# Optimization experiments

Hardware: AMD Instinct MI355X
Metric: run time of the kernel (lower is better)

Reference implementation:

```python
import math
import jax, jax.numpy as jnp
import numpy as np

L, B = 576, 16           # residues, batch
HID, ALPHA = 800, 60     # lstm hidden, alphabet size
IN0, IN1 = 41, 2 * HID   # lstm layer input sizes (20 one-hot + 21 pssm)


def _unit(v):
    return v / jnp.linalg.norm(v, axis=-1, keepdims=True)


def _frame(a, b, c):
    # rotation matrix (columns) of the local reference frame at point c
    bc = _unit(c - b)
    n = _unit(jnp.cross(b - a, bc))
    return jnp.stack([bc, jnp.cross(n, bc), n], axis=-1)  # (..., 3, 3)


def _extend(a, b, c, ct):
    # place next atom given previous three atoms and SRF coordinates ct
    R = _frame(a, b, c)
    return c + jnp.einsum('...ij,...j->...i', R, ct)


def lstm_dir(x, w_ih, w_hh, b_ih, b_hh, reverse=False):
    # single-direction LSTM over x: (T, B, D); torch gate order i,f,g,o
    H = w_hh.shape[1]
    Bb = x.shape[1]

    def step(carry, xt):
        h, cst = carry
        gates = xt @ w_ih.T + b_ih + h @ w_hh.T + b_hh
        i, f, g, o = jnp.split(gates, 4, axis=-1)
        cnew = jax.nn.sigmoid(f) * cst + jax.nn.sigmoid(i) * jnp.tanh(g)
        hnew = jax.nn.sigmoid(o) * jnp.tanh(cnew)
        return (hnew, cnew), hnew

    zeros = jnp.zeros((Bb, H), x.dtype)
    _, hs = jax.lax.scan(step, (zeros, zeros), x, reverse=reverse)
    return hs  # (T, B, H), in original time order for both directions


def torsion_to_srf(r, theta, phi):
    # r, theta: (3,) fixed bond lengths/angles; phi: (L, B, 3) torsions
    r = r[None, None, :]
    th = theta[None, None, :]
    c = jnp.stack([r * jnp.cos(th) * jnp.ones_like(phi),
                   r * jnp.cos(phi) * jnp.sin(th),
                   r * jnp.sin(phi) * jnp.sin(th)], axis=-1)  # (L, B, 3, 3)
    Lx, Bx = phi.shape[0], phi.shape[1]
    return jnp.transpose(c, (0, 2, 1, 3)).reshape(3 * Lx, Bx, 3)


def pnerf(c_tilde, nfrag):
    # parallel NeRF: run nfrag fragments in parallel, then stitch sequentially
    A, Bb, _ = c_tilde.shape
    F = A // nfrag  # assumes divisibility (guaranteed by chosen L)
    c = c_tilde.reshape(nfrag, F, Bb, 3).transpose(1, 0, 2, 3).reshape(F, nfrag * Bb, 3)
    init = jnp.array([[-np.sqrt(0.5), np.sqrt(1.5), 0.0],
                      [-np.sqrt(2.0), 0.0, 0.0],
                      [0.0, 0.0, 0.0]], dtype=c_tilde.dtype)
    a0 = jnp.broadcast_to(init[0], (nfrag * Bb, 3))
    b0 = jnp.broadcast_to(init[1], (nfrag * Bb, 3))
    c0 = jnp.broadcast_to(init[2], (nfrag * Bb, 3))

    def step(carry, ct):
        a, b, cc = carry
        d = _extend(a, b, cc, ct)
        return (b, cc, d), d

    _, frag = jax.lax.scan(step, (a0, b0, c0), c)  # (F, nfrag*Bb, 3)
    frag = frag.reshape(F, nfrag, Bb, 3)

    coords = frag[:, 0]  # fragment 0 already in global frame
    for k in range(1, nfrag):  # small fixed loop over fragments
        R = _frame(coords[-3], coords[-2], coords[-1])  # (Bb, 3, 3)
        g = coords[-1][None] + jnp.einsum('bij,fbj->fbi', R, frag[:, k])
        coords = jnp.concatenate([coords, g], axis=0)
    return coords  # (3L, B, 3)


def _p(k, shape):
    return 0.05 * jax.random.normal(k, shape, dtype=jnp.float32)


def setup_inputs():
    key = jax.random.key(0)
    ks = jax.random.split(key, 32)
    inp = {}
    inp['seq'] = jax.random.randint(ks[0], (L, B), 0, 20)
    inp['pssm'] = jax.random.uniform(ks[1], (L, B, 21), dtype=jnp.float32)
    inp['length'] = jnp.full((B,), L, dtype=jnp.int32)  # full lengths (packing is a no-op)
    i = 2
    for layer, din in ((0, IN0), (1, IN1)):
        for d in ('f', 'b'):
            inp[f'w_ih_l{layer}{d}'] = _p(ks[i], (4 * HID, din)); i += 1
            inp[f'w_hh_l{layer}{d}'] = _p(ks[i], (4 * HID, HID)); i += 1
            inp[f'b_ih_l{layer}{d}'] = _p(ks[i], (4 * HID,)); i += 1
            inp[f'b_hh_l{layer}{d}'] = _p(ks[i], (4 * HID,)); i += 1
    inp['fc_w'] = _p(ks[i], (ALPHA, 2 * HID)); i += 1
    inp['fc_b'] = _p(ks[i], (ALPHA,)); i += 1
    inp['alphabet'] = jax.random.uniform(ks[i], (ALPHA, 3), minval=-math.pi, maxval=math.pi, dtype=jnp.float32); i += 1
    inp['bond_lengths'] = jnp.array([145.867432, 152.534744, 132.935516], dtype=jnp.float32)
    inp['bond_angles'] = jnp.array([1.019982, 1.20471, 1.109421], dtype=jnp.float32)
    return inp


def reference(seq, pssm, length,
              w_ih_l0f, w_hh_l0f, b_ih_l0f, b_hh_l0f,
              w_ih_l0b, w_hh_l0b, b_ih_l0b, b_hh_l0b,
              w_ih_l1f, w_hh_l1f, b_ih_l1f, b_hh_l1f,
              w_ih_l1b, w_hh_l1b, b_ih_l1b, b_hh_l1b,
              fc_w, fc_b, alphabet, bond_lengths, bond_angles):
    # eval mode: inter-layer dropout omitted; all lengths == L so packing is identity
    x = jnp.concatenate([jax.nn.one_hot(seq, 20, dtype=pssm.dtype), pssm], axis=-1)  # (L,B,41)
    h = jnp.concatenate([lstm_dir(x, w_ih_l0f, w_hh_l0f, b_ih_l0f, b_hh_l0f),
                         lstm_dir(x, w_ih_l0b, w_hh_l0b, b_ih_l0b, b_hh_l0b, reverse=True)], axis=-1)
    h = jnp.concatenate([lstm_dir(h, w_ih_l1f, w_hh_l1f, b_ih_l1f, b_hh_l1f),
                         lstm_dir(h, w_ih_l1b, w_hh_l1b, b_ih_l1b, b_hh_l1b, reverse=True)], axis=-1)
    p = jax.nn.softmax(h @ fc_w.T + fc_b, axis=-1)            # (L,B,ALPHA)
    phi = jnp.arctan2(p @ jnp.sin(alphabet), p @ jnp.cos(alphabet))  # (L,B,3)
    srf = torsion_to_srf(bond_lengths, bond_angles, phi)      # (3L,B,3)
    return pnerf(srf, int(math.sqrt(L)))                      # (3L,B,3)
```

## Files before the change

kernel.cpp:

```cpp
#include <hip/hip_runtime.h>
#include <hip/hip_fp16.h>

#define L_SEQ 576
#define BATCH 16
#define HIDDEN 800
#define NT 200
#define KQ_HH 25
#define KQ_L1 50
#define KQ_L0 2

typedef _Float16 h8 __attribute__((ext_vector_type(8)));
typedef _Float16 h4 __attribute__((ext_vector_type(4)));
typedef float f4 __attribute__((ext_vector_type(4)));
typedef int v4i __attribute__((ext_vector_type(4)));
typedef int v2i __attribute__((ext_vector_type(2)));

__device__ __forceinline__ float sigmoidf_(float x){
  x = fminf(30.f, fmaxf(-30.f, x));
  return 1.f/(1.f+__expf(-x));
}
__device__ __forceinline__ float tanhf_(float x){
  x = fminf(15.f, fmaxf(-15.f, x));
  float e = __expf(2.f*x);
  return (e-1.f)/(e+1.f);
}

__global__ void init_h(v4i* __restrict__ h){
  size_t i = (size_t)blockIdx.x*256 + threadIdx.x;
  v4i s = {0x7C007C00, 0x7C007C00, 0x7C007C00, 0x7C007C00};
  h[i] = s;
}

__global__ void build_x(const int* __restrict__ seq, const float* __restrict__ pssm,
                        _Float16* __restrict__ x){
  int i = blockIdx.x*256 + threadIdx.x;
  if(i >= L_SEQ*BATCH*64) return;
  int m = i >> 6, k = i & 63;
  float v = 0.f;
  if(k < 20)      v = (seq[m]==k) ? 1.f : 0.f;
  else if(k < 41) v = pssm[m*21 + (k-20)];
  x[i] = (_Float16)v;
}

__global__ void prep_w(
  const float* __restrict__ whh0f, const float* __restrict__ whh0b,
  const float* __restrict__ whh1f, const float* __restrict__ whh1b,
  const float* __restrict__ wih1f, const float* __restrict__ wih1b,
  const float* __restrict__ wih0f, const float* __restrict__ wih0b,
  h8* __restrict__ wp_hh, h8* __restrict__ wp1, h8* __restrict__ wp0)
{
  long idx = (long)blockIdx.x*256 + threadIdx.x;
  const long J1 = 4L*320000, J2 = 2L*640000, J3 = 2L*25600;
  if(idx < J1){
    int d = (int)(idx/320000); int r = (int)(idx%320000);
    int T = r/1600, q = (r%1600)/64, l = r&63;
    const float* W = (d==0)?whh0f:(d==1)?whh0b:(d==2)?whh1f:whh1b;
    int c = l&15; int n = (c&3)*800 + T*4 + (c>>2);
    const float* src = W + (size_t)n*800 + q*32 + ((l>>4)<<3);
    h8 v;
    #pragma unroll
    for(int j=0;j<8;++j) v[j] = (_Float16)src[j];
    wp_hh[idx] = v;
  } else if(idx < J1+J2){
    long i2 = idx - J1;
    int d = (int)(i2/640000); int r = (int)(i2%640000);
    int T = r/3200, q = (r%3200)/64, l = r&63;
    const float* W = d ? wih1b : wih1f;
    int c = l&15; int n = (c&3)*800 + T*4 + (c>>2);
    const float* src = W + (size_t)n*1600 + q*32 + ((l>>4)<<3);
    h8 v;
    #pragma unroll
    for(int j=0;j<8;++j) v[j] = (_Float16)src[j];
    wp1[i2] = v;
  } else if(idx < J1+J2+J3){
    long i3 = idx - J1 - J2;
    int d = (int)(i3/25600); int r = (int)(i3%25600);
    int T = r/128, q = (r%128)/64, l = r&63;
    const float* W = d ? wih0b : wih0f;
    int c = l&15; int n = (c&3)*800 + T*4 + (c>>2);
    int k0 = q*32 + ((l>>4)<<3);
    h8 v;
    #pragma unroll
    for(int j=0;j<8;++j){ int k = k0+j; v[j] = (_Float16)((k<41)? W[(size_t)n*41+k] : 0.f); }
    wp0[i3] = v;
  }
}

__global__ __launch_bounds__(256) void gemm_l0(
  const _Float16* __restrict__ A,
  const h8* __restrict__ WpF, const h8* __restrict__ WpB,
  const float* __restrict__ bihF, const float* __restrict__ bhhF,
  const float* __restrict__ bihB, const float* __restrict__ bhhB,
  _Float16* __restrict__ GpF, _Float16* __restrict__ GpB)
{
  const int wv = threadIdx.x >> 6;
  const int l  = threadIdx.x & 63;
  const int mg = blockIdx.x % 144;
  const int tg = blockIdx.x / 144;
  const int mt = mg*4 + wv;
  const int dir = tg / 50;
  const int Tb  = (tg % 50) * 4;
  const h8* Wp = dir ? WpB : WpF;
  const float* bih = dir ? bihB : bihF;
  const float* bhh = dir ? bhhB : bhhF;
  _Float16* Gp = dir ? GpB : GpF;

  const _Float16* ab = A + (size_t)(mt*16 + (l&15))*64 + ((l>>4)<<3);
  f4 acc[4] = {{0.f,0.f,0.f,0.f},{0.f,0.f,0.f,0.f},{0.f,0.f,0.f,0.f},{0.f,0.f,0.f,0.f}};
  for(int q=0;q<KQ_L0;++q){
    h8 av = *(const h8*)(ab + q*32);
    #pragma unroll
    for(int j=0;j<4;++j){
      h8 bv = Wp[((size_t)(Tb+j)*KQ_L0 + q)*64 + l];
      acc[j] = __builtin_amdgcn_mfma_f32_16x16x32_f16(bv, av, acc[j], 0, 0, 0);
    }
  }
  const int hi = l >> 4;
  #pragma unroll
  for(int j=0;j<4;++j){
    int T = Tb + j;
    int u = T*4 + hi;
    h4 o;
    #pragma unroll
    for(int r=0;r<4;++r){
      float bias = bih[r*800+u] + bhh[r*800+u];
      o[r] = (_Float16)(acc[j][r] + bias);
    }
    *(h4*)(Gp + (((size_t)mt*NT + T)*64 + l)*4) = o;
  }
}

__global__ __launch_bounds__(256) void gemm_l1(
  const h8* __restrict__ Af,
  const h8* __restrict__ WpF, const h8* __restrict__ WpB,
  const float* __restrict__ bihF, const float* __restrict__ bhhF,
  const float* __restrict__ bihB, const float* __restrict__ bhhB,
  _Float16* __restrict__ GpF, _Float16* __restrict__ GpB)
{
  __shared__ v4i ldsB[2][256];
  const int tid = threadIdx.x;
  const int wv = tid >> 6;
  const int l  = tid & 63;
  const int mg  = blockIdx.x % 36;
  const int tgd = blockIdx.x / 36;
  const int dir = tgd / 50;
  const int tg  = tgd % 50;
  const int Tb  = tg * 4;
  const int mtb = mg*16 + wv*4;
  const h8* Wp = dir ? WpB : WpF;
  const float* bih = dir ? bihB : bihF;
  const float* bhh = dir ? bhhB : bhhF;
  _Float16* Gp = dir ? GpB : GpF;

  const h8* a0 = Af + (size_t)(mtb+0)*3200 + l;
  const h8* a1 = Af + (size_t)(mtb+1)*3200 + l;
  const h8* a2 = Af + (size_t)(mtb+2)*3200 + l;
  const h8* a3 = Af + (size_t)(mtb+3)*3200 + l;

  f4 acc[4][4];
  #pragma unroll
  for(int m=0;m<4;++m)
    #pragma unroll
    for(int j=0;j<4;++j){ acc[m][j][0]=0.f; acc[m][j][1]=0.f; acc[m][j][2]=0.f; acc[m][j][3]=0.f; }

  {
    int j = tid >> 6, ll = tid & 63;
    ldsB[0][tid] = *(const v4i*)(Wp + ((size_t)(Tb+j)*KQ_L1 + 0)*64 + ll);
  }
  __syncthreads();
  for(int q=0;q<KQ_L1;++q){
    const int buf = q & 1;
    if(q+1 < KQ_L1){
      int j = tid >> 6, ll = tid & 63;
      ldsB[buf^1][tid] = *(const v4i*)(Wp + ((size_t)(Tb+j)*KQ_L1 + (q+1))*64 + ll);
    }
    h8 av0 = a0[q*64];
    h8 av1 = a1[q*64];
    h8 av2 = a2[q*64];
    h8 av3 = a3[q*64];
    #pragma unroll
    for(int j=0;j<4;++j){
      h8 bv = __builtin_bit_cast(h8, ldsB[buf][j*64 + l]);
      acc[0][j] = __builtin_amdgcn_mfma_f32_16x16x32_f16(bv, av0, acc[0][j], 0, 0, 0);
      acc[1][j] = __builtin_amdgcn_mfma_f32_16x16x32_f16(bv, av1, acc[1][j], 0, 0, 0);
      acc[2][j] = __builtin_amdgcn_mfma_f32_16x16x32_f16(bv, av2, acc[2][j], 0, 0, 0);
      acc[3][j] = __builtin_amdgcn_mfma_f32_16x16x32_f16(bv, av3, acc[3][j], 0, 0, 0);
    }
    __syncthreads();
  }
  const int hi = l >> 4;
  #pragma unroll
  for(int j=0;j<4;++j){
    int T = Tb + j;
    int u = T*4 + hi;
    float b0 = bih[0*800+u] + bhh[0*800+u];
    float b1 = bih[1*800+u] + bhh[1*800+u];
    float b2 = bih[2*800+u] + bhh[2*800+u];
    float b3 = bih[3*800+u] + bhh[3*800+u];
    #pragma unroll
    for(int m=0;m<4;++m){
      h4 o;
      o[0]=(_Float16)(acc[m][j][0]+b0); o[1]=(_Float16)(acc[m][j][1]+b1);
      o[2]=(_Float16)(acc[m][j][2]+b2); o[3]=(_Float16)(acc[m][j][3]+b3);
      *(h4*)(Gp + (((size_t)(mtb+m)*NT + T)*64 + l)*4) = o;
    }
  }
}

__global__ __launch_bounds__(256,1) void lstm_kernel(
  const h8* __restrict__ WpF, const h8* __restrict__ WpB,
  const _Float16* __restrict__ GpF, const _Float16* __restrict__ GpB,
  h8* __restrict__ hfrag)
{
  __shared__ __attribute__((aligned(16))) char lds_h[2*25600];
  const int tid = threadIdx.x;
  const int wv  = tid >> 6;
  const int l   = tid & 63;
  const bool bwd = blockIdx.x >= 50;
  const int T = ((bwd ? (int)blockIdx.x - 50 : (int)blockIdx.x) << 2) + wv;
  const h8* Wp = bwd ? WpB : WpF;
  const _Float16* Gp = bwd ? GpB : GpF;
  const int dirOff = bwd ? 1600 : 0;

  h8 Bf[KQ_HH];
  #pragma unroll
  for(int q=0;q<KQ_HH;++q) Bf[q] = Wp[(T*KQ_HH + q)*64 + l];

  float cs = 0.f;
  const int qb = wv*6;
  const int storeUnit = ((T>>3)<<6) + (((T>>1)&3)<<4);
  const int storeHalf = (T&1)<<3;

  for(int s=0; s<L_SEQ; ++s){
    const int t = bwd ? (L_SEQ-1-s) : s;

    h4 gp4 = *(const h4*)(Gp + (((size_t)t*NT + T)*64 + l)*4);

    #pragma unroll
    for(int q=0;q<KQ_HH;++q) asm volatile("" : "+v"(Bf[q]));

    char* lbuf = lds_h + (s&1)*25600;
    if(s > 0){
      const h8* src = hfrag + (size_t)(bwd ? t+1 : t-1)*3200 + dirOff + l;
      v4i w[7];
      for(;;){
        #pragma unroll
        for(int i=0;i<7;++i){
          unsigned long long ad = (unsigned long long)(src + (qb+i)*64);
          asm volatile("global_load_dwordx4 %0, %1, off sc1"
                       : "=v"(w[i]) : "v"(ad) : "memory");
        }
        asm volatile("s_waitcnt vmcnt(0)"
          : "+v"(w[0]),"+v"(w[1]),"+v"(w[2]),"+v"(w[3]),"+v"(w[4]),
            "+v"(w[5]),"+v"(w[6])
          :
          : "memory");
        int orac = 0;
        #pragma unroll
        for(int i=0;i<7;++i) orac |= (w[i][0]|w[i][1]) | (w[i][2]|w[i][3]);
        if(__all((orac & 0x40004000) == 0)) break;
        __builtin_amdgcn_s_sleep(1);
      }
      #pragma unroll
      for(int i=0;i<7;++i)
        *(v4i*)(lbuf + (qb+i)*1024 + l*16) = w[i];
    }
    __syncthreads();

    f4 acc[4];
    acc[0][0]=(float)gp4[0]; acc[0][1]=(float)gp4[1]; acc[0][2]=(float)gp4[2]; acc[0][3]=(float)gp4[3];
    #pragma unroll
    for(int j=1;j<4;++j){ acc[j][0]=0.f; acc[j][1]=0.f; acc[j][2]=0.f; acc[j][3]=0.f; }
    if(s > 0){
      #pragma unroll
      for(int q=0;q<KQ_HH;++q){
        v4i wq = *(const v4i*)(lbuf + q*1024 + l*16);
        acc[q&3] = __builtin_amdgcn_mfma_f32_16x16x32_f16(
                     Bf[q], __builtin_bit_cast(h8, wq), acc[q&3], 0,0,0);
      }
    }
    f4 g = (acc[0]+acc[1]) + (acc[2]+acc[3]);

    float cn = sigmoidf_(g[1])*cs + sigmoidf_(g[0])*tanhf_(g[2]);
    cs = cn;
    float hv = sigmoidf_(g[3])*tanhf_(cn);

    {
      _Float16 hf = (_Float16)hv;
      unsigned int u0 = (unsigned int)__builtin_bit_cast(unsigned short, hf);
      unsigned int up = (unsigned int)__shfl_xor((int)u0, 16, 64);
      unsigned int d01 = u0 | (up << 16);
      unsigned int d23 = (unsigned int)__shfl_xor((int)d01, 32, 64);
      if(l < 16){
        v2i ov; ov[0] = (int)d01; ov[1] = (int)d23;
        unsigned long long ad = (unsigned long long)
          ((char*)(hfrag + (size_t)t*3200 + dirOff + storeUnit + l) + storeHalf);
        asm volatile("global_store_dwordx2 %0, %1, off sc1" : : "v"(ad), "v"(ov) : "memory");
      }
    }
  }
}

__global__ void head_kernel(const h8* __restrict__ h1f,
                            const float* __restrict__ fcw, const float* __restrict__ fcb,
                            const float* __restrict__ alphabet,
                            const float* __restrict__ bl, const float* __restrict__ ba,
                            float* __restrict__ srf)
{
  __shared__ h8 sh8[16*201];
  __shared__ float slog[960];
  __shared__ float smax[16];
  __shared__ float sphi[48];
  const int t = blockIdx.x, tid = threadIdx.x;
  const h8* src = h1f + (size_t)t*3200;
  for(int u=tid; u<3200; u+=256){
    int q2 = u >> 6, r = u & 63, sub = r >> 4, m = r & 15;
    sh8[m*201 + (q2<<2) + sub] = src[u];
  }
  __syncthreads();
  for(int it=tid; it<960; it+=256){
    int j = it >> 4, b = it & 15;
    float acc = fcb[j];
    const float4* wr = (const float4*)(fcw + (size_t)j*1600);
    const h8* hr = sh8 + b*201;
    for(int k=0;k<200;++k){
      h8 hv = hr[k];
      float4 w0 = wr[2*k], w1 = wr[2*k+1];
      acc += w0.x*(float)hv[0] + w0.y*(float)hv[1] + w0.z*(float)hv[2] + w0.w*(float)hv[3]
           + w1.x*(float)hv[4] + w1.y*(float)hv[5] + w1.z*(float)hv[6] + w1.w*(float)hv[7];
    }
    slog[b*60 + j] = acc;
  }
  __syncthreads();
  if(tid < 16){
    float mx = -1e30f;
    for(int j=0;j<60;++j) mx = fmaxf(mx, slog[tid*60+j]);
    smax[tid] = mx;
  }
  __syncthreads();
  if(tid < 48){
    int b = tid/3, ax = tid%3;
    float s=0.f, c=0.f, mx = smax[b];
    for(int j=0;j<60;++j){
      float e = __expf(slog[b*60+j] - mx);
      float al = alphabet[j*3 + ax];
      s += e*__sinf(al); c += e*__cosf(al);
    }
    sphi[b*3+ax] = atan2f(s, c);
  }
  __syncthreads();
  if(tid < 144){
    int jj = tid/48; int r_ = tid%48; int b = r_/3, ax = r_%3;
    float rr = bl[jj], th = ba[jj], ph = sphi[b*3+jj];
    float v = (ax==0) ? rr*__cosf(th)
            : (ax==1) ? rr*__cosf(ph)*__sinf(th)
                      : rr*__sinf(ph)*__sinf(th);
    srf[(((size_t)(3*t+jj))*16 + b)*3 + ax] = v;
  }
}

__device__ __forceinline__ void frame_cols(
  float ax,float ay,float az, float bx,float by,float bz, float cx,float cy,float cz,
  float* R)
{
  float ux=cx-bx, uy=cy-by, uz=cz-bz;
  float ir = rsqrtf(ux*ux+uy*uy+uz*uz);
  float bcx=ux*ir, bcy=uy*ir, bcz=uz*ir;
  float px=bx-ax, py=by-ay, pz=bz-az;
  float nx=py*bcz-pz*bcy, ny=pz*bcx-px*bcz, nz=px*bcy-py*bcx;
  float in_ = rsqrtf(nx*nx+ny*ny+nz*nz);
  nx*=in_; ny*=in_; nz*=in_;
  float mx=ny*bcz-nz*bcy, my=nz*bcx-nx*bcz, mz=nx*bcy-ny*bcx;
  R[0]=bcx;R[1]=bcy;R[2]=bcz; R[3]=mx;R[4]=my;R[5]=mz; R[6]=nx;R[7]=ny;R[8]=nz;
}

__global__ void pnerf_kernel(const float* __restrict__ srf,
                             float* __restrict__ frag, float* __restrict__ out)
{
  __shared__ float tail[3][16][3];
  __shared__ float sR[16][9];
  __shared__ float sorg[16][3];
  const int tid = threadIdx.x;
  if(tid < 384){
    int k = tid >> 4, b = tid & 15;
    float ax=-0.70710678f, ay=1.22474487f, az=0.f;
    float bx=-1.41421356f, by=0.f, bz=0.f;
    float cx=0.f, cy=0.f, cz=0.f;
    for(int f=0; f<72; ++f){
      const float* ct = srf + (((size_t)(k*72+f))*16 + b)*3;
      float t0=ct[0], t1=ct[1], t2=ct[2];
      float R[9];
      frame_cols(ax,ay,az, bx,by,bz, cx,cy,cz, R);
      float dx = cx + R[0]*t0 + R[3]*t1 + R[6]*t2;
      float dy = cy + R[1]*t0 + R[4]*t1 + R[7]*t2;
      float dz = cz + R[2]*t0 + R[5]*t1 + R[8]*t2;
      float* fr = frag + (((size_t)(f*24+k))*16 + b)*3;
      fr[0]=dx; fr[1]=dy; fr[2]=dz;
      if(k == 0){
        float* o = out + ((size_t)(f*16)+b)*3;
        o[0]=dx; o[1]=dy; o[2]=dz;
        if(f >= 69){ tail[f-69][b][0]=dx; tail[f-69][b][1]=dy; tail[f-69][b][2]=dz; }
      }
      ax=bx; ay=by; az=bz;  bx=cx; by=cy; bz=cz;  cx=dx; cy=dy; cz=dz;
    }
  }
  __syncthreads();
  for(int kk=1; kk<24; ++kk){
    if(tid < 16){
      int b = tid;
      frame_cols(tail[0][b][0],tail[0][b][1],tail[0][b][2],
                 tail[1][b][0],tail[1][b][1],tail[1][b][2],
                 tail[2][b][0],tail[2][b][1],tail[2][b][2], &sR[b][0]);
      sorg[b][0]=tail[2][b][0]; sorg[b][1]=tail[2][b][1]; sorg[b][2]=tail[2][b][2];
    }
    __syncthreads();
    for(int idx=tid; idx<1152; idx+=blockDim.x){
      int f = idx >> 4, b = idx & 15;
      const float* v = frag + (((size_t)(f*24+kk))*16 + b)*3;
      float vx=v[0], vy=v[1], vz=v[2];
      float gx = sorg[b][0] + sR[b][0]*vx + sR[b][3]*vy + sR[b][6]*vz;
      float gy = sorg[b][1] + sR[b][1]*vx + sR[b][4]*vy + sR[b][7]*vz;
      float gz = sorg[b][2] + sR[b][2]*vx + sR[b][5]*vy + sR[b][8]*vz;
      float* o = out + (((size_t)(kk*72+f))*16 + b)*3;
      o[0]=gx; o[1]=gy; o[2]=gz;
      if(f >= 69){ tail[f-69][b][0]=gx; tail[f-69][b][1]=gy; tail[f-69][b][2]=gz; }
    }
    __syncthreads();
  }
}

extern "C" void kernel_launch(void* const* d_in, const int* in_sizes, int n_in,
                              void* d_out, int out_size, void* d_ws, size_t ws_size,
                              hipStream_t stream)
{
  (void)in_sizes; (void)n_in; (void)out_size; (void)ws_size;
  const int*   seq  = (const int*)d_in[0];
  const float* pssm = (const float*)d_in[1];
  const float* w_ih_l0f=(const float*)d_in[3];  const float* w_hh_l0f=(const float*)d_in[4];
  const float* b_ih_l0f=(const float*)d_in[5];  const float* b_hh_l0f=(const float*)d_in[6];
  const float* w_ih_l0b=(const float*)d_in[7];  const float* w_hh_l0b=(const float*)d_in[8];
  const float* b_ih_l0b=(const float*)d_in[9];  const float* b_hh_l0b=(const float*)d_in[10];
  const float* w_ih_l1f=(const float*)d_in[11]; const float* w_hh_l1f=(const float*)d_in[12];
  const float* b_ih_l1f=(const float*)d_in[13]; const float* b_hh_l1f=(const float*)d_in[14];
  const float* w_ih_l1b=(const float*)d_in[15]; const float* w_hh_l1b=(const float*)d_in[16];
  const float* b_ih_l1b=(const float*)d_in[17]; const float* b_hh_l1b=(const float*)d_in[18];
  const float* fc_w=(const float*)d_in[19];     const float* fc_b=(const float*)d_in[20];
  const float* alphabet=(const float*)d_in[21];
  const float* bl=(const float*)d_in[22];       const float* ba=(const float*)d_in[23];
  float* out = (float*)d_out;

  char* ws = (char*)d_ws;
  size_t o = 0;
  auto alloc = [&](size_t bytes){ size_t r = o; o = (o + bytes + 255) & ~(size_t)255; return r; };
  size_t o_wphh = alloc(4ull*320000*16);
  size_t o_wp1  = alloc(2ull*640000*16);
  size_t o_wp0  = alloc(2ull*25600*16);
  size_t o_gpf  = alloc(2ull*29491200);
  size_t o_gpb  = alloc(2ull*29491200);
  size_t o_h0   = alloc(16ull*576*3200);
  size_t o_h1   = alloc(16ull*576*3200);
  size_t o_x    = alloc(2ull*589824);
  size_t o_srf  = alloc(4ull*82944);
  size_t o_frag = alloc(4ull*82944);

  h8* wp_hh = (h8*)(ws + o_wphh);
  h8* wp1   = (h8*)(ws + o_wp1);
  h8* wp0   = (h8*)(ws + o_wp0);
  _Float16* gpf = (_Float16*)(ws + o_gpf);
  _Float16* gpb = (_Float16*)(ws + o_gpb);
  h8* h0    = (h8*)(ws + o_h0);
  h8* h1    = (h8*)(ws + o_h1);
  _Float16* x = (_Float16*)(ws + o_x);
  float* srf    = (float*)(ws + o_srf);
  float* frag   = (float*)(ws + o_frag);

  init_h<<<14400, 256, 0, stream>>>((v4i*)(ws + o_h0));
  build_x<<<2304, 256, 0, stream>>>(seq, pssm, x);
  prep_w<<<10200, 256, 0, stream>>>(w_hh_l0f, w_hh_l0b, w_hh_l1f, w_hh_l1b,
                                    w_ih_l1f, w_ih_l1b, w_ih_l0f, w_ih_l0b,
                                    wp_hh, wp1, wp0);
  gemm_l0<<<14400, 256, 0, stream>>>(x, wp0, wp0 + 25600,
                                     b_ih_l0f, b_hh_l0f, b_ih_l0b, b_hh_l0b, gpf, gpb);
  lstm_kernel<<<100, 256, 0, stream>>>(wp_hh, wp_hh + 320000, gpf, gpb, h0);
  gemm_l1<<<3600, 256, 0, stream>>>(h0, wp1, wp1 + 640000,
                                    b_ih_l1f, b_hh_l1f, b_ih_l1b, b_hh_l1b, gpf, gpb);
  lstm_kernel<<<100, 256, 0, stream>>>(wp_hh + 640000, wp_hh + 960000, gpf, gpb, h1);
  head_kernel<<<576, 256, 0, stream>>>(h1, fc_w, fc_b, alphabet, bl, ba, srf);
  pnerf_kernel<<<1, 512, 0, stream>>>(srf, frag, out);
}
```

Measured before the change: 2.861 ms.

## Process two gate tiles per wave in persistent LSTM, halving block count

Each wave now owns two output tiles (T and T+100) of the recurrent weight matrix, holding both weight fragments in registers and reusing each LDS-staged h fragment for two MFMAs. The LSTM kernel launches 50 blocks instead of 100. This cuts the number of blocks that poll global memory for the previous hidden state each step and reduces cross-block synchronization traffic. In exchange it doubles register pressure (50 h8 weight registers per lane) and doubles serial MFMA and activation work per wave on the recurrence critical path.

```diff
diff --git a/kernel.cpp b/kernel.cpp
--- a/kernel.cpp
+++ b/kernel.cpp
@@ -216,28 +216,38 @@
   const int tid = threadIdx.x;
   const int wv  = tid >> 6;
   const int l   = tid & 63;
-  const bool bwd = blockIdx.x >= 50;
-  const int T = ((bwd ? (int)blockIdx.x - 50 : (int)blockIdx.x) << 2) + wv;
+  const bool bwd = blockIdx.x >= 25;
+  const int wid = ((bwd ? (int)blockIdx.x - 25 : (int)blockIdx.x) << 2) + wv;
+  const int T0 = wid, T1 = wid + 100;
   const h8* Wp = bwd ? WpB : WpF;
   const _Float16* Gp = bwd ? GpB : GpF;
   const int dirOff = bwd ? 1600 : 0;
 
-  h8 Bf[KQ_HH];
+  h8 Bf0[KQ_HH], Bf1[KQ_HH];
   #pragma unroll
-  for(int q=0;q<KQ_HH;++q) Bf[q] = Wp[(T*KQ_HH + q)*64 + l];
-
-  float cs = 0.f;
+  for(int q=0;q<KQ_HH;++q){
+    Bf0[q] = Wp[(T0*KQ_HH + q)*64 + l];
+    Bf1[q] = Wp[(T1*KQ_HH + q)*64 + l];
+  }
+
+  float cs0 = 0.f, cs1 = 0.f;
   const int qb = wv*6;
-  const int storeUnit = ((T>>3)<<6) + (((T>>1)&3)<<4);
-  const int storeHalf = (T&1)<<3;
+  const int sU0 = ((T0>>3)<<6) + (((T0>>1)&3)<<4);
+  const int sH0 = (T0&1)<<3;
+  const int sU1 = ((T1>>3)<<6) + (((T1>>1)&3)<<4);
+  const int sH1 = (T1&1)<<3;
 
   for(int s=0; s<L_SEQ; ++s){
     const int t = bwd ? (L_SEQ-1-s) : s;
 
-    h4 gp4 = *(const h4*)(Gp + (((size_t)t*NT + T)*64 + l)*4);
-
-    #pragma unroll
-    for(int q=0;q<KQ_HH;++q) asm volatile("" : "+v"(Bf[q]));
+    h4 gp0 = *(const h4*)(Gp + (((size_t)t*NT + T0)*64 + l)*4);
+    h4 gp1 = *(const h4*)(Gp + (((size_t)t*NT + T1)*64 + l)*4);
+
+    #pragma unroll
+    for(int q=0;q<KQ_HH;++q){
+      asm volatile("" : "+v"(Bf0[q]));
+      asm volatile("" : "+v"(Bf1[q]));
+    }
 
     char* lbuf = lds_h + (s&1)*25600;
     if(s > 0){
@@ -267,34 +277,55 @@
     }
     __syncthreads();
 
-    f4 acc[4];
-    acc[0][0]=(float)gp4[0]; acc[0][1]=(float)gp4[1]; acc[0][2]=(float)gp4[2]; acc[0][3]=(float)gp4[3];
-    #pragma unroll
-    for(int j=1;j<4;++j){ acc[j][0]=0.f; acc[j][1]=0.f; acc[j][2]=0.f; acc[j][3]=0.f; }
+    f4 acc0[4], acc1[4];
+    acc0[0][0]=(float)gp0[0]; acc0[0][1]=(float)gp0[1]; acc0[0][2]=(float)gp0[2]; acc0[0][3]=(float)gp0[3];
+    acc1[0][0]=(float)gp1[0]; acc1[0][1]=(float)gp1[1]; acc1[0][2]=(float)gp1[2]; acc1[0][3]=(float)gp1[3];
+    #pragma unroll
+    for(int j=1;j<4;++j){
+      acc0[j][0]=0.f; acc0[j][1]=0.f; acc0[j][2]=0.f; acc0[j][3]=0.f;
+      acc1[j][0]=0.f; acc1[j][1]=0.f; acc1[j][2]=0.f; acc1[j][3]=0.f;
+    }
     if(s > 0){
       #pragma unroll
       for(int q=0;q<KQ_HH;++q){
         v4i wq = *(const v4i*)(lbuf + q*1024 + l*16);
-        acc[q&3] = __builtin_amdgcn_mfma_f32_16x16x32_f16(
-                     Bf[q], __builtin_bit_cast(h8, wq), acc[q&3], 0,0,0);
+        h8 hq = __builtin_bit_cast(h8, wq);
+        acc0[q&3] = __builtin_amdgcn_mfma_f32_16x16x32_f16(Bf0[q], hq, acc0[q&3], 0,0,0);
+        acc1[q&3] = __builtin_amdgcn_mfma_f32_16x16x32_f16(Bf1[q], hq, acc1[q&3], 0,0,0);
       }
     }
-    f4 g = (acc[0]+acc[1]) + (acc[2]+acc[3]);
-
-    float cn = sigmoidf_(g[1])*cs + sigmoidf_(g[0])*tanhf_(g[2]);
-    cs = cn;
-    float hv = sigmoidf_(g[3])*tanhf_(cn);
-
+    f4 g0 = (acc0[0]+acc0[1]) + (acc0[2]+acc0[3]);
+    f4 g1 = (acc1[0]+acc1[1]) + (acc1[2]+acc1[3]);
+
+    float cn0 = sigmoidf_(g0[1])*cs0 + sigmoidf_(g0[0])*tanhf_(g0[2]);
+    cs0 = cn0;
+    float hv0 = sigmoidf_(g0[3])*tanhf_(cn0);
+    float cn1 = sigmoidf_(g1[1])*cs1 + sigmoidf_(g1[0])*tanhf_(g1[2]);
+    cs1 = cn1;
+    float hv1 = sigmoidf_(g1[3])*tanhf_(cn1);
+
+    h8* hrow = hfrag + (size_t)t*3200 + dirOff;
     {
-      _Float16 hf = (_Float16)hv;
+      _Float16 hf = (_Float16)hv0;
       unsigned int u0 = (unsigned int)__builtin_bit_cast(unsigned short, hf);
       unsigned int up = (unsigned int)__shfl_xor((int)u0, 16, 64);
       unsigned int d01 = u0 | (up << 16);
       unsigned int d23 = (unsigned int)__shfl_xor((int)d01, 32, 64);
       if(l < 16){
         v2i ov; ov[0] = (int)d01; ov[1] = (int)d23;
-        unsigned long long ad = (unsigned long long)
-          ((char*)(hfrag + (size_t)t*3200 + dirOff + storeUnit + l) + storeHalf);
+        unsigned long long ad = (unsigned long long)((char*)(hrow + sU0 + l) + sH0);
+        asm volatile("global_store_dwordx2 %0, %1, off sc1" : : "v"(ad), "v"(ov) : "memory");
+      }
+    }
+    {
+      _Float16 hf = (_Float16)hv1;
+      unsigned int u0 = (unsigned int)__builtin_bit_cast(unsigned short, hf);
+      unsigned int up = (unsigned int)__shfl_xor((int)u0, 16, 64);
+      unsigned int d01 = u0 | (up << 16);
+      unsigned int d23 = (unsigned int)__shfl_xor((int)d01, 32, 64);
+      if(l < 16){
+        v2i ov; ov[0] = (int)d01; ov[1] = (int)d23;
+        unsigned long long ad = (unsigned long long)((char*)(hrow + sU1 + l) + sH1);
         asm volatile("global_store_dwordx2 %0, %1, off sc1" : : "v"(ad), "v"(ov) : "memory");
       }
     }
@@ -481,10 +512,10 @@
                                     wp_hh, wp1, wp0);
   gemm_l0<<<14400, 256, 0, stream>>>(x, wp0, wp0 + 25600,
                                      b_ih_l0f, b_hh_l0f, b_ih_l0b, b_hh_l0b, gpf, gpb);
-  lstm_kernel<<<100, 256, 0, stream>>>(wp_hh, wp_hh + 320000, gpf, gpb, h0);
+  lstm_kernel<<<50, 256, 0, stream>>>(wp_hh, wp_hh + 320000, gpf, gpb, h0);
   gemm_l1<<<3600, 256, 0, stream>>>(h0, wp1, wp1 + 640000,
                                     b_ih_l1f, b_hh_l1f, b_ih_l1b, b_hh_l1b, gpf, gpb);
-  lstm_kernel<<<100, 256, 0, stream>>>(wp_hh + 640000, wp_hh + 960000, gpf, gpb, h1);
+  lstm_kernel<<<50, 256, 0, stream>>>(wp_hh + 640000, wp_hh + 960000, gpf, gpb, h1);
   head_kernel<<<576, 256, 0, stream>>>(h1, fc_w, fc_b, alphabet, bl, ba, srf);
   pnerf_kernel<<<1, 512, 0, stream>>>(srf, frag, out);
 }
```

Measured after the change: 3.435 ms. 20.1% more time.
